# Kernel tuning notes

Measured on AMD Instinct MI355X. Metric: run time of the kernel, lower is better.

Reference implementation:

```python
import jax, jax.numpy as jnp
import numpy as np

D_MODEL = 2048
N_HEADS = 16
HEAD_DIM = D_MODEL // N_HEADS


def setup_inputs() -> dict:
    key = jax.random.key(0)
    ks = jax.random.split(key, 5)
    scale = 1.0 / np.sqrt(D_MODEL)
    x = jax.random.normal(ks[0], (2, 2048, D_MODEL), dtype=jnp.float32)
    W_qkv = jax.random.normal(ks[1], (D_MODEL, 3 * D_MODEL), dtype=jnp.float32) * scale
    b_qkv = jnp.zeros((3 * D_MODEL,), dtype=jnp.float32)
    W_out = jax.random.normal(ks[2], (D_MODEL, D_MODEL), dtype=jnp.float32) * scale
    b_out = jnp.zeros((D_MODEL,), dtype=jnp.float32)
    return {"x": x, "W_qkv": W_qkv, "b_qkv": b_qkv, "W_out": W_out, "b_out": b_out}


def reference(x, W_qkv, b_qkv, W_out, b_out):
    bsz, seq_len, _ = x.shape
    # QKV projection: (b, s, 3*d) -> (3, b, h, s, hd)
    qkv = x @ W_qkv + b_qkv
    qkv = qkv.reshape(bsz, seq_len, 3, N_HEADS, HEAD_DIM)
    qkv = jnp.transpose(qkv, (2, 0, 3, 1, 4))
    q, k, v = qkv[0], qkv[1], qkv[2]
    # scaled dot-product scores: (b, h, s, s)
    scores = jnp.einsum("bhqd,bhkd->bhqk", q, k) / np.sqrt(HEAD_DIM).astype(np.float32)
    causal = jnp.tril(jnp.ones((seq_len, seq_len), dtype=bool))
    scores = jnp.where(causal[None, None], scores, -jnp.inf)
    attn = jax.nn.softmax(scores, axis=-1)
    # attention output: (b, h, s, hd) -> (b, s, d)
    out = jnp.einsum("bhqk,bhkd->bhqd", attn, v)
    out = jnp.transpose(out, (0, 2, 1, 3)).reshape(bsz, seq_len, D_MODEL)
    y = out @ W_out + b_out
    return y
```

## Files before the change

kernel.cpp:

```cpp
#include <hip/hip_runtime.h>
#include <stdint.h>
#include <stddef.h>


typedef __attribute__((ext_vector_type(8))) short bf16x8;
typedef __attribute__((ext_vector_type(4))) float f32x4;

#define SOFT_SCALE 0.12751743075419806f

__device__ __forceinline__ short f2bf(float f) {
  union { float f; unsigned u; } v; v.f = f;
  unsigned u = v.u + 0x7fffu + ((v.u >> 16) & 1u);
  return (short)(u >> 16);
}

__device__ __forceinline__ void gload_lds16(const void* g, const void* l) {
  __builtin_amdgcn_global_load_lds(
      (__attribute__((address_space(1))) void*)(uintptr_t)g,
      (__attribute__((address_space(3))) void*)(uintptr_t)l,
      16, 0, 0);
}

__global__ __launch_bounds__(256) void cast_f32_bf16(
    const float* __restrict__ in, short* __restrict__ out, int n8) {
  int i = blockIdx.x * 256 + threadIdx.x;
  if (i >= n8) return;
  float4 a = ((const float4*)in)[i * 2];
  float4 b = ((const float4*)in)[i * 2 + 1];
  bf16x8 o;
  o[0] = f2bf(a.x); o[1] = f2bf(a.y); o[2] = f2bf(a.z); o[3] = f2bf(a.w);
  o[4] = f2bf(b.x); o[5] = f2bf(b.y); o[6] = f2bf(b.z); o[7] = f2bf(b.w);
  ((bf16x8*)out)[i] = o;
}

__global__ __launch_bounds__(256) void transpose_cast_w(
    const float* __restrict__ W, short* __restrict__ WT, int K, int N) {
  __shared__ short t[32][33];
  int k0 = blockIdx.x * 32, n0 = blockIdx.y * 32;
  int r = threadIdx.x >> 3;
  int c = (threadIdx.x & 7) * 4;
  float4 v = *(const float4*)(W + (size_t)(k0 + r) * N + n0 + c);
  t[r][c + 0] = f2bf(v.x); t[r][c + 1] = f2bf(v.y);
  t[r][c + 2] = f2bf(v.z); t[r][c + 3] = f2bf(v.w);
  __syncthreads();
  short4 o;
  o.x = t[c + 0][r]; o.y = t[c + 1][r]; o.z = t[c + 2][r]; o.w = t[c + 3][r];
  *(short4*)(WT + (size_t)(n0 + r) * K + k0 + c) = o;
}

__global__ __launch_bounds__(256) void transpose_v(
    const short* __restrict__ qkv, short* __restrict__ vT) {
  __shared__ short t[64][72];
  int bh = blockIdx.z, b = bh >> 4, h = bh & 15;
  int s0 = blockIdx.x * 64, d0 = blockIdx.y * 64;
  const short* src = qkv + (size_t)b * 2048 * 6144 + 4096 + h * 128 + d0;
  short* dst = vT + (size_t)bh * 128 * 2048;
#pragma unroll
  for (int it = 0; it < 2; ++it) {
    int e = threadIdx.x * 8 + it * 2048;
    int sr = e >> 6, sc = e & 63;
    bf16x8 v = *(const bf16x8*)(src + (size_t)(s0 + sr) * 6144 + sc);
#pragma unroll
    for (int j = 0; j < 8; ++j) t[sr][sc + j] = v[j];
  }
  __syncthreads();
#pragma unroll
  for (int it = 0; it < 2; ++it) {
    int e = threadIdx.x * 8 + it * 2048;
    int dr = e >> 6, dc = e & 63;
    bf16x8 o;
#pragma unroll
    for (int j = 0; j < 8; ++j) o[j] = t[dc + j][dr];
    *(bf16x8*)(dst + (size_t)(d0 + dr) * 2048 + s0 + dc) = o;
  }
}

template <int BF16OUT>
__global__ __launch_bounds__(256) void gemm_bt(
    const short* __restrict__ A, const short* __restrict__ BT,
    void* __restrict__ Cv, const float* __restrict__ bias,
    int M, int N, int K) {
  __shared__ __align__(16) short As[128 * 32];
  __shared__ __align__(16) short Bs[128 * 32];
  const int tid = threadIdx.x;
  const int wave = tid >> 6, lane = tid & 63;
  const int quad = lane >> 4, l16 = lane & 15;
  const int wm = (wave >> 1) * 64, wn = (wave & 1) * 64;
  const int m0 = blockIdx.x * 128, n0 = blockIdx.y * 128;

  f32x4 acc[4][4] = {};

  for (int k0 = 0; k0 < K; k0 += 32) {
    __syncthreads();
#pragma unroll
    for (int it = 0; it < 2; ++it) {
      int e = tid * 8 + it * 2048;
      int r = e >> 5, c = e & 31;
      gload_lds16(A + (size_t)(m0 + r) * K + k0 + c,
                  (const char*)As + it * 4096 + wave * 1024);
    }
#pragma unroll
    for (int it = 0; it < 2; ++it) {
      int e = tid * 8 + it * 2048;
      int r = e >> 5, c = e & 31;
      gload_lds16(BT + (size_t)(n0 + r) * K + k0 + c,
                  (const char*)Bs + it * 4096 + wave * 1024);
    }
    __syncthreads();
    bf16x8 af[4], bfg[4];
#pragma unroll
    for (int t = 0; t < 4; ++t)
      af[t] = *(const bf16x8*)(As + (wm + t * 16 + l16) * 32 + quad * 8);
#pragma unroll
    for (int t = 0; t < 4; ++t)
      bfg[t] = *(const bf16x8*)(Bs + (wn + t * 16 + l16) * 32 + quad * 8);
#pragma unroll
    for (int tm = 0; tm < 4; ++tm)
#pragma unroll
      for (int tn = 0; tn < 4; ++tn)
        acc[tm][tn] = __builtin_amdgcn_mfma_f32_16x16x32_bf16(
            af[tm], bfg[tn], acc[tm][tn], 0, 0, 0);
  }

#pragma unroll
  for (int tn = 0; tn < 4; ++tn) {
    int n = n0 + wn + tn * 16 + l16;
    float bv = bias[n];
#pragma unroll
    for (int tm = 0; tm < 4; ++tm) {
      int mb = m0 + wm + tm * 16 + quad * 4;
#pragma unroll
      for (int r = 0; r < 4; ++r) {
        float v = acc[tm][tn][r] + bv;
        if (BF16OUT)
          ((short*)Cv)[(size_t)(mb + r) * N + n] = f2bf(v);
        else
          ((float*)Cv)[(size_t)(mb + r) * N + n] = v;
      }
    }
  }
}

__global__ __launch_bounds__(256, 2) void attn_kernel(
    const short* __restrict__ qkv, const short* __restrict__ vT,
    short* __restrict__ obuf) {
  __shared__ __align__(16) short Ks[16384];
  __shared__ __align__(16) short Vs[16384];
  const int tid = threadIdx.x;
  const int wave = tid >> 6, lane = tid & 63;
  const int quad = lane >> 4, l16 = lane & 15;
  const int bh = blockIdx.y, b = bh >> 4, h = bh & 15;
  const int pp = blockIdx.x;

  const short* qbase = qkv + (size_t)b * 2048 * 6144 + h * 128;
  const short* kbase = qkv + (size_t)b * 2048 * 6144 + 2048 + h * 128;
  const short* vtbase = vT + (size_t)bh * 128 * 2048;
  short* obase = obuf + (size_t)b * 2048 * 2048 + h * 128;

  const int srow = lane >> 2;
  const int scol = (lane & 3) * 8;

  for (int half = 0; half < 2; ++half) {
    const int p = half ? (31 - pp) : pp;
    const int q0 = p * 64;
    const int nkt = (p >> 1) + 1;

    bf16x8 qf[4];
#pragma unroll
    for (int kk = 0; kk < 4; ++kk)
      qf[kk] = *(const bf16x8*)(
          qbase + (size_t)(q0 + wave * 16 + l16) * 6144 + kk * 32 + quad * 8);

    f32x4 acco[8] = {};
    float mrun[4], lrun[4];
#pragma unroll
    for (int r = 0; r < 4; ++r) { mrun[r] = -1e30f; lrun[r] = 0.f; }

    for (int kt = 0; kt < nkt; ++kt) {
      const int k0 = kt * 128;
      __syncthreads();
#pragma unroll
      for (int it = 0; it < 8; ++it) {
        gload_lds16(
            kbase + (size_t)(k0 + it * 16 + srow) * 6144 + wave * 32 + scol,
            (const char*)Ks + (wave * 8 + it) * 1024);
      }
#pragma unroll
      for (int it = 0; it < 8; ++it) {
        gload_lds16(
            vtbase + (size_t)(it * 16 + srow) * 2048 + k0 + wave * 32 + scol,
            (const char*)Vs + (wave * 8 + it) * 1024);
      }
      __syncthreads();

      f32x4 accs[8] = {};
#pragma unroll
      for (int kk = 0; kk < 4; ++kk) {
        bf16x8 bfg[8];
#pragma unroll
        for (int tn = 0; tn < 8; ++tn)
          bfg[tn] = *(const bf16x8*)((const char*)Ks + (kk * 8 + tn) * 1024 +
                                     l16 * 64 + quad * 16);
#pragma unroll
        for (int tn = 0; tn < 8; ++tn)
          accs[tn] = __builtin_amdgcn_mfma_f32_16x16x32_bf16(
              qf[kk], bfg[tn], accs[tn], 0, 0, 0);
      }

      const bool diag = (kt == nkt - 1);
#pragma unroll
      for (int tn = 0; tn < 8; ++tn)
#pragma unroll
        for (int r = 0; r < 4; ++r) {
          float s = accs[tn][r] * SOFT_SCALE;
          if (diag) {
            int grow = q0 + wave * 16 + quad * 4 + r;
            int gcol = k0 + tn * 16 + l16;
            if (gcol > grow) s = -1e30f;
          }
          accs[tn][r] = s;
        }

#pragma unroll
      for (int r = 0; r < 4; ++r) {
        float mx = accs[0][r];
#pragma unroll
        for (int tn = 1; tn < 8; ++tn) mx = fmaxf(mx, accs[tn][r]);
#pragma unroll
        for (int off = 1; off < 16; off <<= 1)
          mx = fmaxf(mx, __shfl_xor(mx, off, 64));
        float mn = fmaxf(mrun[r], mx);
        float al = exp2f(mrun[r] - mn);
        mrun[r] = mn;
        float rs = 0.f;
#pragma unroll
        for (int tn = 0; tn < 8; ++tn) {
          float pv = exp2f(accs[tn][r] - mn);
          accs[tn][r] = pv;
          rs += pv;
        }
#pragma unroll
        for (int off = 1; off < 16; off <<= 1)
          rs += __shfl_xor(rs, off, 64);
        lrun[r] = lrun[r] * al + rs;
#pragma unroll
        for (int tn = 0; tn < 8; ++tn) acco[tn][r] *= al;
      }

      __syncthreads();

#pragma unroll
      for (int r = 0; r < 4; ++r) {
        int row = wave * 16 + quad * 4 + r;
#pragma unroll
        for (int tn = 0; tn < 8; ++tn)
          Ks[row * 136 + tn * 16 + l16] = f2bf(accs[tn][r]);
      }

#pragma unroll
      for (int kk = 0; kk < 4; ++kk) {
        bf16x8 av = *(const bf16x8*)(Ks + (wave * 16 + l16) * 136 + kk * 32 +
                                     quad * 8);
        bf16x8 bfg[8];
#pragma unroll
        for (int tn = 0; tn < 8; ++tn)
          bfg[tn] = *(const bf16x8*)((const char*)Vs + (kk * 8 + tn) * 1024 +
                                     l16 * 64 + quad * 16);
#pragma unroll
        for (int tn = 0; tn < 8; ++tn)
          acco[tn] = __builtin_amdgcn_mfma_f32_16x16x32_bf16(
              av, bfg[tn], acco[tn], 0, 0, 0);
      }
    }

    float inv[4];
#pragma unroll
    for (int r = 0; r < 4; ++r) inv[r] = 1.f / lrun[r];
#pragma unroll
    for (int r = 0; r < 4; ++r) {
      int row = q0 + wave * 16 + quad * 4 + r;
#pragma unroll
      for (int tn = 0; tn < 8; ++tn)
        obase[(size_t)row * 2048 + tn * 16 + l16] = f2bf(acco[tn][r] * inv[r]);
    }
  }
}

extern "C" void kernel_launch(void* const* d_in, const int* in_sizes, int n_in,
                              void* d_out, int out_size, void* d_ws,
                              size_t ws_size, hipStream_t stream) {
  (void)in_sizes; (void)n_in; (void)out_size; (void)ws_size;
  const float* x    = (const float*)d_in[0];
  const float* Wqkv = (const float*)d_in[1];
  const float* bqkv = (const float*)d_in[2];
  const float* Wout = (const float*)d_in[3];
  const float* bout = (const float*)d_in[4];
  float* out = (float*)d_out;

  char* ws = (char*)d_ws;
  short* xb    = (short*)(ws);
  short* wqkvT = (short*)(ws + 16777216);
  short* woutT = (short*)(ws + 41943040);
  short* qkv   = (short*)(ws + 50331648);
  short* vTb   = (short*)(ws + 100663296);
  short* obuf  = (short*)(ws + 117440512);

  cast_f32_bf16<<<4096, 256, 0, stream>>>(x, xb, 1048576);
  transpose_cast_w<<<dim3(64, 192), 256, 0, stream>>>(Wqkv, wqkvT, 2048, 6144);
  transpose_cast_w<<<dim3(64, 64), 256, 0, stream>>>(Wout, woutT, 2048, 2048);

  gemm_bt<1><<<dim3(32, 48), 256, 0, stream>>>(xb, wqkvT, (void*)qkv, bqkv,
                                               4096, 6144, 2048);

  transpose_v<<<dim3(32, 2, 32), 256, 0, stream>>>(qkv, vTb);

  attn_kernel<<<dim3(16, 32), 256, 0, stream>>>(qkv, vTb, obuf);

  gemm_bt<0><<<dim3(32, 16), 256, 0, stream>>>(obuf, woutT, (void*)out, bout,
                                               4096, 2048, 2048);
}
```

Baseline: 434.2 us.

## Deepen GEMM K-tile to 64 and split attention into one block per query tile

```diff
diff --git a/kernel.cpp b/kernel.cpp
--- a/kernel.cpp
+++ b/kernel.cpp
@@ -80,55 +80,67 @@
     const short* __restrict__ A, const short* __restrict__ BT,
     void* __restrict__ Cv, const float* __restrict__ bias,
     int M, int N, int K) {
-  __shared__ __align__(16) short As[128 * 32];
-  __shared__ __align__(16) short Bs[128 * 32];
+  __shared__ __align__(16) short As[128 * 64];
+  __shared__ __align__(16) short Bs[128 * 64];
   const int tid = threadIdx.x;
   const int wave = tid >> 6, lane = tid & 63;
   const int quad = lane >> 4, l16 = lane & 15;
-  const int wm = (wave >> 1) * 64, wn = (wave & 1) * 64;
+  const int wmg = (wave >> 1) * 4;
+  const int wng = (wave & 1) * 4;
   const int m0 = blockIdx.x * 128, n0 = blockIdx.y * 128;
+  const int srow = lane >> 2;
+  const int scol = (lane & 3) * 8;
+
+  const short* aptr[4];
+  const short* bptr[4];
+#pragma unroll
+  for (int it = 0; it < 4; ++it) {
+    int c = wave * 4 + it;
+    int row = (c >> 1) * 16 + srow, col = (c & 1) * 32 + scol;
+    aptr[it] = A + (size_t)(m0 + row) * K + col;
+    bptr[it] = BT + (size_t)(n0 + row) * K + col;
+  }
 
   f32x4 acc[4][4] = {};
 
-  for (int k0 = 0; k0 < K; k0 += 32) {
-    __syncthreads();
-#pragma unroll
-    for (int it = 0; it < 2; ++it) {
-      int e = tid * 8 + it * 2048;
-      int r = e >> 5, c = e & 31;
-      gload_lds16(A + (size_t)(m0 + r) * K + k0 + c,
-                  (const char*)As + it * 4096 + wave * 1024);
-    }
-#pragma unroll
-    for (int it = 0; it < 2; ++it) {
-      int e = tid * 8 + it * 2048;
-      int r = e >> 5, c = e & 31;
-      gload_lds16(BT + (size_t)(n0 + r) * K + k0 + c,
-                  (const char*)Bs + it * 4096 + wave * 1024);
-    }
-    __syncthreads();
-    bf16x8 af[4], bfg[4];
-#pragma unroll
-    for (int t = 0; t < 4; ++t)
-      af[t] = *(const bf16x8*)(As + (wm + t * 16 + l16) * 32 + quad * 8);
-#pragma unroll
-    for (int t = 0; t < 4; ++t)
-      bfg[t] = *(const bf16x8*)(Bs + (wn + t * 16 + l16) * 32 + quad * 8);
-#pragma unroll
-    for (int tm = 0; tm < 4; ++tm)
-#pragma unroll
-      for (int tn = 0; tn < 4; ++tn)
-        acc[tm][tn] = __builtin_amdgcn_mfma_f32_16x16x32_bf16(
-            af[tm], bfg[tn], acc[tm][tn], 0, 0, 0);
+  for (int k0 = 0; k0 < K; k0 += 64) {
+    __syncthreads();
+#pragma unroll
+    for (int it = 0; it < 4; ++it)
+      gload_lds16(aptr[it], (const char*)As + (wave * 4 + it) * 1024);
+#pragma unroll
+    for (int it = 0; it < 4; ++it)
+      gload_lds16(bptr[it], (const char*)Bs + (wave * 4 + it) * 1024);
+#pragma unroll
+    for (int it = 0; it < 4; ++it) { aptr[it] += 64; bptr[it] += 64; }
+    __syncthreads();
+#pragma unroll
+    for (int kk = 0; kk < 2; ++kk) {
+      bf16x8 af[4], bfg[4];
+#pragma unroll
+      for (int t = 0; t < 4; ++t)
+        af[t] = *(const bf16x8*)(As + ((wmg + t) * 2 + kk) * 512 + l16 * 32 +
+                                 quad * 8);
+#pragma unroll
+      for (int t = 0; t < 4; ++t)
+        bfg[t] = *(const bf16x8*)(Bs + ((wng + t) * 2 + kk) * 512 + l16 * 32 +
+                                  quad * 8);
+#pragma unroll
+      for (int tm = 0; tm < 4; ++tm)
+#pragma unroll
+        for (int tn = 0; tn < 4; ++tn)
+          acc[tm][tn] = __builtin_amdgcn_mfma_f32_16x16x32_bf16(
+              af[tm], bfg[tn], acc[tm][tn], 0, 0, 0);
+    }
   }
 
 #pragma unroll
   for (int tn = 0; tn < 4; ++tn) {
-    int n = n0 + wn + tn * 16 + l16;
+    int n = n0 + (wng + tn) * 16 + l16;
     float bv = bias[n];
 #pragma unroll
     for (int tm = 0; tm < 4; ++tm) {
-      int mb = m0 + wm + tm * 16 + quad * 4;
+      int mb = m0 + (wmg + tm) * 16 + quad * 4;
 #pragma unroll
       for (int r = 0; r < 4; ++r) {
         float v = acc[tm][tn][r] + bv;
@@ -141,7 +153,7 @@
   }
 }
 
-__global__ __launch_bounds__(256, 2) void attn_kernel(
+__global__ __launch_bounds__(256, 4) void attn_kernel(
     const short* __restrict__ qkv, const short* __restrict__ vT,
     short* __restrict__ obuf) {
   __shared__ __align__(16) short Ks[16384];
@@ -150,7 +162,9 @@
   const int wave = tid >> 6, lane = tid & 63;
   const int quad = lane >> 4, l16 = lane & 15;
   const int bh = blockIdx.y, b = bh >> 4, h = bh & 15;
-  const int pp = blockIdx.x;
+  const int p = blockIdx.x;
+  const int q0 = p * 64;
+  const int nkt = (p >> 1) + 1;
 
   const short* qbase = qkv + (size_t)b * 2048 * 6144 + h * 128;
   const short* kbase = qkv + (size_t)b * 2048 * 6144 + 2048 + h * 128;
@@ -160,129 +174,123 @@
   const int srow = lane >> 2;
   const int scol = (lane & 3) * 8;
 
-  for (int half = 0; half < 2; ++half) {
-    const int p = half ? (31 - pp) : pp;
-    const int q0 = p * 64;
-    const int nkt = (p >> 1) + 1;
-
-    bf16x8 qf[4];
-#pragma unroll
-    for (int kk = 0; kk < 4; ++kk)
-      qf[kk] = *(const bf16x8*)(
-          qbase + (size_t)(q0 + wave * 16 + l16) * 6144 + kk * 32 + quad * 8);
-
-    f32x4 acco[8] = {};
-    float mrun[4], lrun[4];
-#pragma unroll
-    for (int r = 0; r < 4; ++r) { mrun[r] = -1e30f; lrun[r] = 0.f; }
-
-    for (int kt = 0; kt < nkt; ++kt) {
-      const int k0 = kt * 128;
-      __syncthreads();
-#pragma unroll
-      for (int it = 0; it < 8; ++it) {
-        gload_lds16(
-            kbase + (size_t)(k0 + it * 16 + srow) * 6144 + wave * 32 + scol,
-            (const char*)Ks + (wave * 8 + it) * 1024);
+  bf16x8 qf[4];
+#pragma unroll
+  for (int kk = 0; kk < 4; ++kk)
+    qf[kk] = *(const bf16x8*)(
+        qbase + (size_t)(q0 + wave * 16 + l16) * 6144 + kk * 32 + quad * 8);
+
+  f32x4 acco[8] = {};
+  float mrun[4], lrun[4];
+#pragma unroll
+  for (int r = 0; r < 4; ++r) { mrun[r] = -1e30f; lrun[r] = 0.f; }
+
+  for (int kt = 0; kt < nkt; ++kt) {
+    const int k0 = kt * 128;
+    __syncthreads();
+#pragma unroll
+    for (int it = 0; it < 8; ++it) {
+      gload_lds16(
+          kbase + (size_t)(k0 + it * 16 + srow) * 6144 + wave * 32 + scol,
+          (const char*)Ks + (wave * 8 + it) * 1024);
+    }
+#pragma unroll
+    for (int it = 0; it < 8; ++it) {
+      gload_lds16(
+          vtbase + (size_t)(it * 16 + srow) * 2048 + k0 + wave * 32 + scol,
+          (const char*)Vs + (wave * 8 + it) * 1024);
+    }
+    __syncthreads();
+
+    f32x4 accs[8] = {};
+#pragma unroll
+    for (int kk = 0; kk < 4; ++kk) {
+      bf16x8 bfg[8];
+#pragma unroll
+      for (int tn = 0; tn < 8; ++tn)
+        bfg[tn] = *(const bf16x8*)((const char*)Ks + (kk * 8 + tn) * 1024 +
+                                   l16 * 64 + quad * 16);
+#pragma unroll
+      for (int tn = 0; tn < 8; ++tn)
+        accs[tn] = __builtin_amdgcn_mfma_f32_16x16x32_bf16(
+            qf[kk], bfg[tn], accs[tn], 0, 0, 0);
+    }
+
+    const bool diag = (kt == nkt - 1);
+#pragma unroll
+    for (int tn = 0; tn < 8; ++tn)
+#pragma unroll
+      for (int r = 0; r < 4; ++r) {
+        float s = accs[tn][r] * SOFT_SCALE;
+        if (diag) {
+          int grow = q0 + wave * 16 + quad * 4 + r;
+          int gcol = k0 + tn * 16 + l16;
+          if (gcol > grow) s = -1e30f;
+        }
+        accs[tn][r] = s;
       }
-#pragma unroll
-      for (int it = 0; it < 8; ++it) {
-        gload_lds16(
-            vtbase + (size_t)(it * 16 + srow) * 2048 + k0 + wave * 32 + scol,
-            (const char*)Vs + (wave * 8 + it) * 1024);
+
+#pragma unroll
+    for (int r = 0; r < 4; ++r) {
+      float mx = accs[0][r];
+#pragma unroll
+      for (int tn = 1; tn < 8; ++tn) mx = fmaxf(mx, accs[tn][r]);
+#pragma unroll
+      for (int off = 1; off < 16; off <<= 1)
+        mx = fmaxf(mx, __shfl_xor(mx, off, 64));
+      float mn = fmaxf(mrun[r], mx);
+      float al = exp2f(mrun[r] - mn);
+      mrun[r] = mn;
+      float rs = 0.f;
+#pragma unroll
+      for (int tn = 0; tn < 8; ++tn) {
+        float pv = exp2f(accs[tn][r] - mn);
+        accs[tn][r] = pv;
+        rs += pv;
       }
-      __syncthreads();
-
-      f32x4 accs[8] = {};
-#pragma unroll
-      for (int kk = 0; kk < 4; ++kk) {
-        bf16x8 bfg[8];
-#pragma unroll
-        for (int tn = 0; tn < 8; ++tn)
-          bfg[tn] = *(const bf16x8*)((const char*)Ks + (kk * 8 + tn) * 1024 +
-                                     l16 * 64 + quad * 16);
-#pragma unroll
-        for (int tn = 0; tn < 8; ++tn)
-          accs[tn] = __builtin_amdgcn_mfma_f32_16x16x32_bf16(
-              qf[kk], bfg[tn], accs[tn], 0, 0, 0);
-      }
-
-      const bool diag = (kt == nkt - 1);
-#pragma unroll
-      for (int tn = 0; tn < 8; ++tn)
-#pragma unroll
-        for (int r = 0; r < 4; ++r) {
-          float s = accs[tn][r] * SOFT_SCALE;
-          if (diag) {
-            int grow = q0 + wave * 16 + quad * 4 + r;
-            int gcol = k0 + tn * 16 + l16;
-            if (gcol > grow) s = -1e30f;
-          }
-          accs[tn][r] = s;
-        }
-
-#pragma unroll
-      for (int r = 0; r < 4; ++r) {
-        float mx = accs[0][r];
-#pragma unroll
-        for (int tn = 1; tn < 8; ++tn) mx = fmaxf(mx, accs[tn][r]);
-#pragma unroll
-        for (int off = 1; off < 16; off <<= 1)
-          mx = fmaxf(mx, __shfl_xor(mx, off, 64));
-        float mn = fmaxf(mrun[r], mx);
-        float al = exp2f(mrun[r] - mn);
-        mrun[r] = mn;
-        float rs = 0.f;
-#pragma unroll
-        for (int tn = 0; tn < 8; ++tn) {
-          float pv = exp2f(accs[tn][r] - mn);
-          accs[tn][r] = pv;
-          rs += pv;
-        }
-#pragma unroll
-        for (int off = 1; off < 16; off <<= 1)
-          rs += __shfl_xor(rs, off, 64);
-        lrun[r] = lrun[r] * al + rs;
-#pragma unroll
-        for (int tn = 0; tn < 8; ++tn) acco[tn][r] *= al;
-      }
-
-      __syncthreads();
-
-#pragma unroll
-      for (int r = 0; r < 4; ++r) {
-        int row = wave * 16 + quad * 4 + r;
-#pragma unroll
-        for (int tn = 0; tn < 8; ++tn)
-          Ks[row * 136 + tn * 16 + l16] = f2bf(accs[tn][r]);
-      }
-
-#pragma unroll
-      for (int kk = 0; kk < 4; ++kk) {
-        bf16x8 av = *(const bf16x8*)(Ks + (wave * 16 + l16) * 136 + kk * 32 +
-                                     quad * 8);
-        bf16x8 bfg[8];
-#pragma unroll
-        for (int tn = 0; tn < 8; ++tn)
-          bfg[tn] = *(const bf16x8*)((const char*)Vs + (kk * 8 + tn) * 1024 +
-                                     l16 * 64 + quad * 16);
-#pragma unroll
-        for (int tn = 0; tn < 8; ++tn)
-          acco[tn] = __builtin_amdgcn_mfma_f32_16x16x32_bf16(
-              av, bfg[tn], acco[tn], 0, 0, 0);
-      }
-    }
-
-    float inv[4];
-#pragma unroll
-    for (int r = 0; r < 4; ++r) inv[r] = 1.f / lrun[r];
+#pragma unroll
+      for (int off = 1; off < 16; off <<= 1)
+        rs += __shfl_xor(rs, off, 64);
+      lrun[r] = lrun[r] * al + rs;
+#pragma unroll
+      for (int tn = 0; tn < 8; ++tn) acco[tn][r] *= al;
+    }
+
+    __syncthreads();
+
 #pragma unroll
     for (int r = 0; r < 4; ++r) {
-      int row = q0 + wave * 16 + quad * 4 + r;
-#pragma unroll
-      for (int tn = 0; tn < 8; ++tn)
-        obase[(size_t)row * 2048 + tn * 16 + l16] = f2bf(acco[tn][r] * inv[r]);
-    }
+      int row = wave * 16 + quad * 4 + r;
+#pragma unroll
+      for (int tn = 0; tn < 8; ++tn)
+        Ks[row * 136 + tn * 16 + l16] = f2bf(accs[tn][r]);
+    }
+
+#pragma unroll
+    for (int kk = 0; kk < 4; ++kk) {
+      bf16x8 av = *(const bf16x8*)(Ks + (wave * 16 + l16) * 136 + kk * 32 +
+                                   quad * 8);
+      bf16x8 bfg[8];
+#pragma unroll
+      for (int tn = 0; tn < 8; ++tn)
+        bfg[tn] = *(const bf16x8*)((const char*)Vs + (kk * 8 + tn) * 1024 +
+                                   l16 * 64 + quad * 16);
+#pragma unroll
+      for (int tn = 0; tn < 8; ++tn)
+        acco[tn] = __builtin_amdgcn_mfma_f32_16x16x32_bf16(
+            av, bfg[tn], acco[tn], 0, 0, 0);
+    }
+  }
+
+  float inv[4];
+#pragma unroll
+  for (int r = 0; r < 4; ++r) inv[r] = 1.f / lrun[r];
+#pragma unroll
+  for (int r = 0; r < 4; ++r) {
+    int row = q0 + wave * 16 + quad * 4 + r;
+#pragma unroll
+    for (int tn = 0; tn < 8; ++tn)
+      obase[(size_t)row * 2048 + tn * 16 + l16] = f2bf(acco[tn][r] * inv[r]);
   }
 }
 
@@ -314,7 +322,7 @@
 
   transpose_v<<<dim3(32, 2, 32), 256, 0, stream>>>(qkv, vTb);
 
-  attn_kernel<<<dim3(16, 32), 256, 0, stream>>>(qkv, vTb, obuf);
+  attn_kernel<<<dim3(32, 32), 256, 0, stream>>>(qkv, vTb, obuf);
 
   gemm_bt<0><<<dim3(32, 16), 256, 0, stream>>>(obuf, woutT, (void*)out, bout,
                                                4096, 2048, 2048);
```

Measured after the change: 558.9 us. 1.29x slower.
